# Optimization experiments

Measured on AMD Instinct MI355X. Metric: run time of the kernel, lower is better.

Reference implementation:

```python
import jax, jax.numpy as jnp
import numpy as np

B, N, M, F, K = 32, 256, 64, 128, 64
N_INTERACT_RES, N_ATOM_RES = 3, 2


def ssp(x):
    # shifted softplus, PhysNet activation
    return jax.nn.softplus(x) - jnp.log(2.0).astype(x.dtype)


def res_block(h, W1, b1, W2, b2):
    # PhysNet residual layer: h + W2 @ ssp(W1 @ ssp(h) + b1) + b2
    t = ssp(h)
    t = ssp(t @ W1.T + b1)
    return h + t @ W2.T + b2


def setup_inputs() -> dict:
    key = jax.random.key(0)
    ks = jax.random.split(key, 20)
    sF = 1.0 / np.sqrt(F)
    sK = 1.0 / np.sqrt(K)
    return {
        "x": jax.random.normal(ks[0], (B, N, F), jnp.float32),
        "rbf": jax.random.uniform(ks[1], (B, N, M, K), jnp.float32),
        "neighbor": jax.random.randint(ks[2], (B, N, M), 0, N, jnp.int32),
        "k2f_W": jax.random.normal(ks[3], (F, K), jnp.float32) * sK,  # no bias
        "Wi": jax.random.normal(ks[4], (F, F), jnp.float32) * sF,
        "bi": jnp.zeros((F,), jnp.float32),
        "ires_W1": jax.random.normal(ks[5], (N_INTERACT_RES, F, F), jnp.float32) * sF,
        "ires_b1": jnp.zeros((N_INTERACT_RES, F), jnp.float32),
        "ires_W2": jax.random.normal(ks[6], (N_INTERACT_RES, F, F), jnp.float32) * sF,
        "ires_b2": jnp.zeros((N_INTERACT_RES, F), jnp.float32),
        "Wint": jax.random.normal(ks[7], (F, F), jnp.float32) * sF,
        "bint": jnp.zeros((F,), jnp.float32),
        "u_gate": jnp.ones((F,), jnp.float32),
        "ares_W1": jax.random.normal(ks[8], (N_ATOM_RES, F, F), jnp.float32) * sF,
        "ares_b1": jnp.zeros((N_ATOM_RES, F), jnp.float32),
        "ares_W2": jax.random.normal(ks[9], (N_ATOM_RES, F, F), jnp.float32) * sF,
        "ares_b2": jnp.zeros((N_ATOM_RES, F), jnp.float32),
    }


def reference(x, rbf, neighbor, k2f_W, Wi, bi, ires_W1, ires_b1, ires_W2, ires_b2,
              Wint, bint, u_gate, ares_W1, ares_b1, ares_W2, ares_b2):
    b, n, f = x.shape
    m = neighbor.shape[2]
    xa = ssp(x)                                            # (B,N,F)
    g = jnp.einsum('bnmk,fk->bnmf', rbf, k2f_W)            # RBF filter (B,N,M,F)
    xi = ssp(xa @ Wi.T + bi)                               # self message
    # gather neighbor features: xj[b,n,m,:] = xa[b, neighbor[b,n,m], :]
    idx = jnp.broadcast_to(neighbor.reshape(b, n * m)[:, :, None], (b, n * m, f))
    xj = jnp.take_along_axis(xa, idx, axis=1).reshape(b, n, m, f)
    xj = jnp.sum(xj * g, axis=2)                           # aggregate over neighbors
    v = xi + xj
    for l in range(ires_W1.shape[0]):
        v = res_block(v, ires_W1[l], ires_b1[l], ires_W2[l], ires_b2[l])
    v = ssp(v)
    out = u_gate * x + (v @ Wint.T + bint)
    for l in range(ares_W1.shape[0]):
        out = res_block(out, ares_W1[l], ares_b1[l], ares_W2[l], ares_b2[l])
    return out
```

## Files before the change

kernel.cpp:

```cpp
#include <hip/hip_runtime.h>
#include <math.h>

#define PB 32
#define PN 256
#define PM 64
#define PF 128
#define PK 64
#define ROWS (PB*PN)
#define NTOT (ROWS*PF)

#define OFF_K2F  0
#define OFF_WI   8192
#define OFF_IW1  24576
#define OFF_IW2  73728
#define OFF_WINT 122880
#define OFF_AW1  139264
#define OFF_AW2  172032
#define TOTAL_W  204800

#define XPITCH 136

typedef __attribute__((ext_vector_type(4))) float  floatx4;
typedef __attribute__((ext_vector_type(8))) short  shortx8;

__device__ __forceinline__ unsigned short f2b(float f){
    union { float f; unsigned int i; } c; c.f = f;
    unsigned int x = c.i;
    return (unsigned short)((x + 0x7fffu + ((x >> 16) & 1u)) >> 16);
}
__device__ __forceinline__ float bf2f(unsigned short u){
    union { unsigned int i; float f; } c; c.i = ((unsigned int)u) << 16; return c.f;
}
__device__ __forceinline__ float sspf(float x){
    return fmaxf(x, 0.0f) + log1pf(expf(-fabsf(x))) - 0.69314718055994531f;
}
__device__ __forceinline__ shortx8 pack8(float4 a, float4 b){
    shortx8 r;
    r[0]=(short)f2b(a.x); r[1]=(short)f2b(a.y); r[2]=(short)f2b(a.z); r[3]=(short)f2b(a.w);
    r[4]=(short)f2b(b.x); r[5]=(short)f2b(b.y); r[6]=(short)f2b(b.z); r[7]=(short)f2b(b.w);
    return r;
}

__global__ __launch_bounds__(256) void k_pre(const float* __restrict__ x,
                                             const float* __restrict__ k2f,
                                             const float* __restrict__ Wi,
                                             const float* __restrict__ iW1,
                                             const float* __restrict__ iW2,
                                             const float* __restrict__ Wint,
                                             const float* __restrict__ aW1,
                                             const float* __restrict__ aW2,
                                             unsigned short* __restrict__ xa_b,
                                             unsigned short* __restrict__ Wb){
    int i = blockIdx.x * 256 + threadIdx.x;
    if (i < NTOT){ xa_b[i] = f2b(sspf(x[i])); return; }
    int j = i - NTOT;
    if (j >= TOTAL_W) return;
    float v;
    if      (j < OFF_WI)   v = k2f[j - OFF_K2F];
    else if (j < OFF_IW1)  v = Wi[j - OFF_WI];
    else if (j < OFF_IW2)  v = iW1[j - OFF_IW1];
    else if (j < OFF_WINT) v = iW2[j - OFF_IW2];
    else if (j < OFF_AW1)  v = Wint[j - OFF_WINT];
    else if (j < OFF_AW2)  v = aW1[j - OFF_AW1];
    else                   v = aW2[j - OFF_AW2];
    Wb[j] = f2b(v);
}

__global__ __launch_bounds__(256) void k_msg(const float* __restrict__ rbf,
                                             const int* __restrict__ nbr,
                                             const unsigned short* __restrict__ Wk2f,
                                             const unsigned short* __restrict__ xa_b,
                                             float* __restrict__ xj){
    const int bid  = blockIdx.x;
    const int b    = bid >> 8;
    const int tid  = threadIdx.x;
    const int wave = tid >> 6;
    const int lane = tid & 63;
    const int quad = lane >> 4;
    const int l16  = lane & 15;

    __shared__ unsigned short Xn[PM * XPITCH];
    __shared__ float xjpart[4][PF];

    const float* rrow = rbf + (size_t)bid * (PM*PK) + (size_t)(wave*16 + l16) * PK;
    shortx8 afrag0 = pack8(*(const float4*)(rrow + quad*8),
                           *(const float4*)(rrow + quad*8 + 4));
    shortx8 afrag1 = pack8(*(const float4*)(rrow + 32 + quad*8),
                           *(const float4*)(rrow + 32 + quad*8 + 4));

    {
        const int r = tid >> 2;
        const int p = tid & 3;
        const int row = nbr[bid*PM + r];
        const uint4* gsrc = (const uint4*)(xa_b + ((size_t)b*PN + row)*PF) + p*4;
        uint4* ldst = (uint4*)((char*)Xn + r*(XPITCH*2) + p*64);
        #pragma unroll
        for (int j = 0; j < 4; ++j) ldst[j] = gsrc[j];
    }
    __syncthreads();

    float s[8];
    #pragma unroll
    for (int ft = 0; ft < 8; ++ft) s[ft] = 0.f;

    #pragma unroll
    for (int ft = 0; ft < 8; ++ft){
        const unsigned short* wrow = Wk2f + (size_t)(ft*16 + l16) * PK;
        shortx8 b0 = *(const shortx8*)(wrow +  0 + quad*8);
        shortx8 b1 = *(const shortx8*)(wrow + 32 + quad*8);
        floatx4 acc = {0.f, 0.f, 0.f, 0.f};
        acc = __builtin_amdgcn_mfma_f32_16x16x32_bf16(afrag0, b0, acc, 0, 0, 0);
        acc = __builtin_amdgcn_mfma_f32_16x16x32_bf16(afrag1, b1, acc, 0, 0, 0);
        #pragma unroll
        for (int r = 0; r < 4; ++r){
            float xv = bf2f(Xn[(wave*16 + quad*4 + r)*XPITCH + ft*16 + l16]);
            s[ft] += acc[r] * xv;
        }
    }
    #pragma unroll
    for (int ft = 0; ft < 8; ++ft){
        float v = s[ft];
        v += __shfl_xor(v, 16, 64);
        v += __shfl_xor(v, 32, 64);
        if (quad == 0) xjpart[wave][ft*16 + l16] = v;
    }
    __syncthreads();
    if (tid < PF){
        float v = xjpart[0][tid] + xjpart[1][tid] + xjpart[2][tid] + xjpart[3][tid];
        xj[(size_t)bid*PF + tid] = v;
    }
}

__device__ __forceinline__ void gemm2(const unsigned short* __restrict__ W,
                                      int l16, int quad, int ftbase,
                                      const shortx8 a[4], floatx4 acc[2]){
    #pragma unroll
    for (int f = 0; f < 2; ++f){
        const unsigned short* wrow = W + (size_t)((ftbase+f)*16 + l16) * PF;
        floatx4 c = {0.f, 0.f, 0.f, 0.f};
        #pragma unroll
        for (int ks = 0; ks < 4; ++ks){
            shortx8 bf = *(const shortx8*)(wrow + ks*32 + quad*8);
            c = __builtin_amdgcn_mfma_f32_16x16x32_bf16(a[ks], bf, c, 0, 0, 0);
        }
        acc[f] = c;
    }
}

__device__ __forceinline__ void relayout(unsigned short* Tls,
                                         const unsigned short t16[8],
                                         int l16, int quad, int ftbase,
                                         shortx8 a[4]){
    __syncthreads();
    #pragma unroll
    for (int f = 0; f < 2; ++f)
        #pragma unroll
        for (int r = 0; r < 4; ++r)
            Tls[(quad*4 + r)*XPITCH + (ftbase+f)*16 + l16] = t16[f*4 + r];
    __syncthreads();
    #pragma unroll
    for (int ks = 0; ks < 4; ++ks)
        a[ks] = *(const shortx8*)(Tls + l16*XPITCH + ks*32 + quad*8);
}

__global__ __launch_bounds__(256) void k_chain(const unsigned short* __restrict__ xa_b,
                                               const float* __restrict__ xj,
                                               const float* __restrict__ x,
                                               const unsigned short* __restrict__ Wb,
                                               const float* __restrict__ bi,
                                               const float* __restrict__ ib1,
                                               const float* __restrict__ ib2,
                                               const float* __restrict__ bint,
                                               const float* __restrict__ ugate,
                                               const float* __restrict__ ab1,
                                               const float* __restrict__ ab2,
                                               float* __restrict__ out){
    const int tid  = threadIdx.x;
    const int wave = tid >> 6;
    const int lane = tid & 63;
    const int quad = lane >> 4;
    const int l16  = lane & 15;
    const int ftb  = wave*2;
    const int row0 = blockIdx.x * 16;

    __shared__ unsigned short Tls[16 * XPITCH];

    int col[2];
    #pragma unroll
    for (int f = 0; f < 2; ++f) col[f] = (ftb+f)*16 + l16;

    const unsigned short* inrow = xa_b + (size_t)(row0 + l16) * PF;
    shortx8 a[4];
    #pragma unroll
    for (int ks = 0; ks < 4; ++ks)
        a[ks] = *(const shortx8*)(inrow + ks*32 + quad*8);

    floatx4 acc[2];
    float V[8];
    unsigned short t16[8];

    gemm2(Wb + OFF_WI, l16, quad, ftb, a, acc);
    #pragma unroll
    for (int f = 0; f < 2; ++f)
        #pragma unroll
        for (int r = 0; r < 4; ++r){
            size_t idx = (size_t)(row0 + quad*4 + r)*PF + col[f];
            float of = sspf(acc[f][r] + bi[col[f]]) + xj[idx];
            V[f*4+r] = of;
            t16[f*4+r] = f2b(sspf(of));
        }
    relayout(Tls, t16, l16, quad, ftb, a);

    for (int l = 0; l < 3; ++l){
        gemm2(Wb + OFF_IW1 + l*PF*PF, l16, quad, ftb, a, acc);
        #pragma unroll
        for (int f = 0; f < 2; ++f)
            #pragma unroll
            for (int r = 0; r < 4; ++r)
                t16[f*4+r] = f2b(sspf(acc[f][r] + ib1[l*PF + col[f]]));
        relayout(Tls, t16, l16, quad, ftb, a);

        gemm2(Wb + OFF_IW2 + l*PF*PF, l16, quad, ftb, a, acc);
        #pragma unroll
        for (int f = 0; f < 2; ++f)
            #pragma unroll
            for (int r = 0; r < 4; ++r){
                V[f*4+r] += acc[f][r] + ib2[l*PF + col[f]];
                t16[f*4+r] = f2b(sspf(V[f*4+r]));
            }
        relayout(Tls, t16, l16, quad, ftb, a);
    }

    gemm2(Wb + OFF_WINT, l16, quad, ftb, a, acc);
    #pragma unroll
    for (int f = 0; f < 2; ++f)
        #pragma unroll
        for (int r = 0; r < 4; ++r){
            size_t idx = (size_t)(row0 + quad*4 + r)*PF + col[f];
            float o = ugate[col[f]] * x[idx] + acc[f][r] + bint[col[f]];
            V[f*4+r] = o;
            t16[f*4+r] = f2b(sspf(o));
        }
    relayout(Tls, t16, l16, quad, ftb, a);

    #pragma unroll
    for (int l = 0; l < 2; ++l){
        gemm2(Wb + OFF_AW1 + l*PF*PF, l16, quad, ftb, a, acc);
        #pragma unroll
        for (int f = 0; f < 2; ++f)
            #pragma unroll
            for (int r = 0; r < 4; ++r)
                t16[f*4+r] = f2b(sspf(acc[f][r] + ab1[l*PF + col[f]]));
        relayout(Tls, t16, l16, quad, ftb, a);

        gemm2(Wb + OFF_AW2 + l*PF*PF, l16, quad, ftb, a, acc);
        if (l == 0){
            #pragma unroll
            for (int f = 0; f < 2; ++f)
                #pragma unroll
                for (int r = 0; r < 4; ++r){
                    V[f*4+r] += acc[f][r] + ab2[l*PF + col[f]];
                    t16[f*4+r] = f2b(sspf(V[f*4+r]));
                }
            relayout(Tls, t16, l16, quad, ftb, a);
        } else {
            #pragma unroll
            for (int f = 0; f < 2; ++f)
                #pragma unroll
                for (int r = 0; r < 4; ++r){
                    size_t idx = (size_t)(row0 + quad*4 + r)*PF + col[f];
                    out[idx] = V[f*4+r] + acc[f][r] + ab2[l*PF + col[f]];
                }
        }
    }
}

extern "C" void kernel_launch(void* const* d_in, const int* in_sizes, int n_in,
                              void* d_out, int out_size, void* d_ws, size_t ws_size,
                              hipStream_t stream){
    const float* x     = (const float*)d_in[0];
    const float* rbf   = (const float*)d_in[1];
    const int*   nbr   = (const int*)d_in[2];
    const float* k2fW  = (const float*)d_in[3];
    const float* Wi    = (const float*)d_in[4];
    const float* bi    = (const float*)d_in[5];
    const float* iW1   = (const float*)d_in[6];
    const float* ib1   = (const float*)d_in[7];
    const float* iW2   = (const float*)d_in[8];
    const float* ib2   = (const float*)d_in[9];
    const float* Wint  = (const float*)d_in[10];
    const float* bint  = (const float*)d_in[11];
    const float* ugate = (const float*)d_in[12];
    const float* aW1   = (const float*)d_in[13];
    const float* ab1   = (const float*)d_in[14];
    const float* aW2   = (const float*)d_in[15];
    const float* ab2   = (const float*)d_in[16];

    char* ws = (char*)d_ws;
    unsigned short* xa_b = (unsigned short*)ws;
    float*          xj   = (float*)(ws + (2ull << 20));
    unsigned short* Wb   = (unsigned short*)(ws + (6ull << 20));

    k_pre<<<(NTOT + TOTAL_W + 255)/256, 256, 0, stream>>>(
        x, k2fW, Wi, iW1, iW2, Wint, aW1, aW2, xa_b, Wb);
    k_msg<<<PB*PN, 256, 0, stream>>>(rbf, nbr, Wb + OFF_K2F, xa_b, xj);
    k_chain<<<ROWS/16, 256, 0, stream>>>(xa_b, xj, x, Wb,
                                         bi, ib1, ib2, bint, ugate, ab1, ab2,
                                         (float*)d_out);
}
```

Baseline: 323.2 us.

## Map one atom per wave in message kernel and double-buffer chain relayout

The message kernel now assigns one atom per wave instead of one per block. It gathers neighbor features straight from a new fp32 copy of ssp(x) through shuffled neighbor indices, which removes the LDS staging, the block barriers and the cross-wave reduction. The chain kernel ping-pongs between two LDS buffers so relayout can drop its leading barrier. In exchange, the pre kernel writes an extra fp32 activation array, and the gather becomes uncoalesced global loads of 4-byte elements, which may raise memory traffic.

Result: faster. 316.1 us (-2.2%).

```diff
diff --git a/kernel.cpp b/kernel.cpp
--- a/kernel.cpp
+++ b/kernel.cpp
@@ -49,10 +49,16 @@
                                              const float* __restrict__ Wint,
                                              const float* __restrict__ aW1,
                                              const float* __restrict__ aW2,
+                                             float* __restrict__ xa_f,
                                              unsigned short* __restrict__ xa_b,
                                              unsigned short* __restrict__ Wb){
     int i = blockIdx.x * 256 + threadIdx.x;
-    if (i < NTOT){ xa_b[i] = f2b(sspf(x[i])); return; }
+    if (i < NTOT){
+        float v = sspf(x[i]);
+        xa_f[i] = v;
+        xa_b[i] = f2b(v);
+        return;
+    }
     int j = i - NTOT;
     if (j >= TOTAL_W) return;
     float v;
@@ -69,65 +75,60 @@
 __global__ __launch_bounds__(256) void k_msg(const float* __restrict__ rbf,
                                              const int* __restrict__ nbr,
                                              const unsigned short* __restrict__ Wk2f,
-                                             const unsigned short* __restrict__ xa_b,
+                                             const float* __restrict__ xa_f,
                                              float* __restrict__ xj){
-    const int bid  = blockIdx.x;
+    const int tid  = threadIdx.x;
+    const int bid  = blockIdx.x * 4 + (tid >> 6);
     const int b    = bid >> 8;
-    const int tid  = threadIdx.x;
-    const int wave = tid >> 6;
     const int lane = tid & 63;
     const int quad = lane >> 4;
     const int l16  = lane & 15;
 
-    __shared__ unsigned short Xn[PM * XPITCH];
-    __shared__ float xjpart[4][PF];
-
-    const float* rrow = rbf + (size_t)bid * (PM*PK) + (size_t)(wave*16 + l16) * PK;
-    shortx8 afrag0 = pack8(*(const float4*)(rrow + quad*8),
-                           *(const float4*)(rrow + quad*8 + 4));
-    shortx8 afrag1 = pack8(*(const float4*)(rrow + 32 + quad*8),
-                           *(const float4*)(rrow + 32 + quad*8 + 4));
-
-    {
-        const int r = tid >> 2;
-        const int p = tid & 3;
-        const int row = nbr[bid*PM + r];
-        const uint4* gsrc = (const uint4*)(xa_b + ((size_t)b*PN + row)*PF) + p*4;
-        uint4* ldst = (uint4*)((char*)Xn + r*(XPITCH*2) + p*64);
-        #pragma unroll
-        for (int j = 0; j < 4; ++j) ldst[j] = gsrc[j];
-    }
-    __syncthreads();
+    const int nbv = nbr[bid*PM + lane];
+    const float* xab = xa_f + (size_t)b * PN * PF;
 
     float s[8];
     #pragma unroll
     for (int ft = 0; ft < 8; ++ft) s[ft] = 0.f;
 
-    #pragma unroll
-    for (int ft = 0; ft < 8; ++ft){
-        const unsigned short* wrow = Wk2f + (size_t)(ft*16 + l16) * PK;
-        shortx8 b0 = *(const shortx8*)(wrow +  0 + quad*8);
-        shortx8 b1 = *(const shortx8*)(wrow + 32 + quad*8);
-        floatx4 acc = {0.f, 0.f, 0.f, 0.f};
-        acc = __builtin_amdgcn_mfma_f32_16x16x32_bf16(afrag0, b0, acc, 0, 0, 0);
-        acc = __builtin_amdgcn_mfma_f32_16x16x32_bf16(afrag1, b1, acc, 0, 0, 0);
-        #pragma unroll
-        for (int r = 0; r < 4; ++r){
-            float xv = bf2f(Xn[(wave*16 + quad*4 + r)*XPITCH + ft*16 + l16]);
-            s[ft] += acc[r] * xv;
-        }
-    }
+    const float* rbase = rbf + (size_t)bid * (PM*PK);
+
+    #pragma unroll
+    for (int t = 0; t < 4; ++t){
+        const float* rrow = rbase + (size_t)(t*16 + l16) * PK;
+        shortx8 afrag0 = pack8(*(const float4*)(rrow + quad*8),
+                               *(const float4*)(rrow + quad*8 + 4));
+        shortx8 afrag1 = pack8(*(const float4*)(rrow + 32 + quad*8),
+                               *(const float4*)(rrow + 32 + quad*8 + 4));
+
+        const int mb = t*16 + quad*4;
+        int idx0 = __shfl(nbv, mb + 0, 64);
+        int idx1 = __shfl(nbv, mb + 1, 64);
+        int idx2 = __shfl(nbv, mb + 2, 64);
+        int idx3 = __shfl(nbv, mb + 3, 64);
+
+        #pragma unroll
+        for (int ft = 0; ft < 8; ++ft){
+            const unsigned short* wrow = Wk2f + (size_t)(ft*16 + l16) * PK;
+            shortx8 b0 = *(const shortx8*)(wrow +  0 + quad*8);
+            shortx8 b1 = *(const shortx8*)(wrow + 32 + quad*8);
+            floatx4 acc = {0.f, 0.f, 0.f, 0.f};
+            acc = __builtin_amdgcn_mfma_f32_16x16x32_bf16(afrag0, b0, acc, 0, 0, 0);
+            acc = __builtin_amdgcn_mfma_f32_16x16x32_bf16(afrag1, b1, acc, 0, 0, 0);
+            const int col = ft*16 + l16;
+            s[ft] += acc[0] * xab[(size_t)idx0*PF + col];
+            s[ft] += acc[1] * xab[(size_t)idx1*PF + col];
+            s[ft] += acc[2] * xab[(size_t)idx2*PF + col];
+            s[ft] += acc[3] * xab[(size_t)idx3*PF + col];
+        }
+    }
+
     #pragma unroll
     for (int ft = 0; ft < 8; ++ft){
         float v = s[ft];
         v += __shfl_xor(v, 16, 64);
         v += __shfl_xor(v, 32, 64);
-        if (quad == 0) xjpart[wave][ft*16 + l16] = v;
-    }
-    __syncthreads();
-    if (tid < PF){
-        float v = xjpart[0][tid] + xjpart[1][tid] + xjpart[2][tid] + xjpart[3][tid];
-        xj[(size_t)bid*PF + tid] = v;
+        if (quad == 0) xj[(size_t)bid*PF + ft*16 + l16] = v;
     }
 }
 
@@ -151,7 +152,6 @@
                                          const unsigned short t16[8],
                                          int l16, int quad, int ftbase,
                                          shortx8 a[4]){
-    __syncthreads();
     #pragma unroll
     for (int f = 0; f < 2; ++f)
         #pragma unroll
@@ -183,7 +183,8 @@
     const int ftb  = wave*2;
     const int row0 = blockIdx.x * 16;
 
-    __shared__ unsigned short Tls[16 * XPITCH];
+    __shared__ unsigned short Tls[2][16 * XPITCH];
+    int p = 0;
 
     int col[2];
     #pragma unroll
@@ -209,7 +210,7 @@
             V[f*4+r] = of;
             t16[f*4+r] = f2b(sspf(of));
         }
-    relayout(Tls, t16, l16, quad, ftb, a);
+    relayout(Tls[p], t16, l16, quad, ftb, a); p ^= 1;
 
     for (int l = 0; l < 3; ++l){
         gemm2(Wb + OFF_IW1 + l*PF*PF, l16, quad, ftb, a, acc);
@@ -218,7 +219,7 @@
             #pragma unroll
             for (int r = 0; r < 4; ++r)
                 t16[f*4+r] = f2b(sspf(acc[f][r] + ib1[l*PF + col[f]]));
-        relayout(Tls, t16, l16, quad, ftb, a);
+        relayout(Tls[p], t16, l16, quad, ftb, a); p ^= 1;
 
         gemm2(Wb + OFF_IW2 + l*PF*PF, l16, quad, ftb, a, acc);
         #pragma unroll
@@ -228,7 +229,7 @@
                 V[f*4+r] += acc[f][r] + ib2[l*PF + col[f]];
                 t16[f*4+r] = f2b(sspf(V[f*4+r]));
             }
-        relayout(Tls, t16, l16, quad, ftb, a);
+        relayout(Tls[p], t16, l16, quad, ftb, a); p ^= 1;
     }
 
     gemm2(Wb + OFF_WINT, l16, quad, ftb, a, acc);
@@ -241,7 +242,7 @@
             V[f*4+r] = o;
             t16[f*4+r] = f2b(sspf(o));
         }
-    relayout(Tls, t16, l16, quad, ftb, a);
+    relayout(Tls[p], t16, l16, quad, ftb, a); p ^= 1;
 
     #pragma unroll
     for (int l = 0; l < 2; ++l){
@@ -251,7 +252,7 @@
             #pragma unroll
             for (int r = 0; r < 4; ++r)
                 t16[f*4+r] = f2b(sspf(acc[f][r] + ab1[l*PF + col[f]]));
-        relayout(Tls, t16, l16, quad, ftb, a);
+        relayout(Tls[p], t16, l16, quad, ftb, a); p ^= 1;
 
         gemm2(Wb + OFF_AW2 + l*PF*PF, l16, quad, ftb, a, acc);
         if (l == 0){
@@ -262,7 +263,7 @@
                     V[f*4+r] += acc[f][r] + ab2[l*PF + col[f]];
                     t16[f*4+r] = f2b(sspf(V[f*4+r]));
                 }
-            relayout(Tls, t16, l16, quad, ftb, a);
+            relayout(Tls[p], t16, l16, quad, ftb, a); p ^= 1;
         } else {
             #pragma unroll
             for (int f = 0; f < 2; ++f)
@@ -298,12 +299,13 @@
 
     char* ws = (char*)d_ws;
     unsigned short* xa_b = (unsigned short*)ws;
-    float*          xj   = (float*)(ws + (2ull << 20));
-    unsigned short* Wb   = (unsigned short*)(ws + (6ull << 20));
+    float*          xa_f = (float*)(ws + (2ull  << 20));
+    float*          xj   = (float*)(ws + (6ull  << 20));
+    unsigned short* Wb   = (unsigned short*)(ws + (10ull << 20));
 
     k_pre<<<(NTOT + TOTAL_W + 255)/256, 256, 0, stream>>>(
-        x, k2fW, Wi, iW1, iW2, Wint, aW1, aW2, xa_b, Wb);
-    k_msg<<<PB*PN, 256, 0, stream>>>(rbf, nbr, Wb + OFF_K2F, xa_b, xj);
+        x, k2fW, Wi, iW1, iW2, Wint, aW1, aW2, xa_f, xa_b, Wb);
+    k_msg<<<ROWS/4, 256, 0, stream>>>(rbf, nbr, Wb + OFF_K2F, xa_f, xj);
     k_chain<<<ROWS/16, 256, 0, stream>>>(xa_b, xj, x, Wb,
                                          bi, ib1, ib2, bint, ugate, ab1, ab2,
                                          (float*)d_out);
```
